# Optimization experiments

Hardware: AMD Instinct MI355X
Metric: run time of the kernel (lower is better)

The kernel has to match this reference:

```python
import jax, jax.numpy as jnp
import numpy as np

N_NODES = 50000
N_EDGES = 600000
N_COMM = 500
COMM_EDGES = 8000
NFEAT = 128
NHID = 128
NCLASS = 10
NLAYERS = 3
NHEADS = 8
EPS = 1e-5


def setup_inputs() -> dict:
    key = jax.random.key(0)
    ks = jax.random.split(key, 32)
    s = 0.05
    def rn(i, shape, scale=s):
        return (jax.random.normal(ks[i], shape, dtype=jnp.float32) * scale)
    return {
        "node_features": jax.random.normal(ks[0], (N_NODES, NFEAT), dtype=jnp.float32),
        "node_edge_index": jax.random.randint(ks[1], (2, N_EDGES), 0, N_NODES),
        "comm_features": jax.random.normal(ks[2], (N_COMM, NHID), dtype=jnp.float32),
        "comm_edge_index": jax.random.randint(ks[3], (2, COMM_EDGES), 0, N_COMM),
        "node_to_comm_map": jax.random.randint(ks[4], (N_NODES,), 0, N_COMM),
        # node-branch GCN params (nfeat == nhid so weights stack)
        "node_W": rn(5, (NLAYERS, NHID, NHID)),
        "node_b": rn(6, (NLAYERS, NHID)),
        "node_bn_g": 1.0 + rn(7, (NLAYERS, NHID)),
        "node_bn_b": rn(8, (NLAYERS, NHID)),
        # community-branch GCN params
        "comm_W": rn(9, (NLAYERS, NHID, NHID)),
        "comm_b": rn(10, (NLAYERS, NHID)),
        "comm_bn_g": 1.0 + rn(11, (NLAYERS, NHID)),
        "comm_bn_b": rn(12, (NLAYERS, NHID)),
        # MultiheadAttention params (torch layout: y = x @ W.T + b)
        "attn_in_w": rn(13, (3 * NHID, NHID)),
        "attn_in_b": rn(14, (3 * NHID,)),
        "attn_out_w": rn(15, (NHID, NHID)),
        "attn_out_b": rn(16, (NHID,)),
        # gate LayerNorm
        "ln_g": 1.0 + rn(17, (NHID,)),
        "ln_b": rn(18, (NHID,)),
        # classifier: Linear(128,64) -> BN -> ReLU -> Linear(64,10)
        "cls_W1": rn(19, (NHID, NHID // 2)),
        "cls_b1": rn(20, (NHID // 2,)),
        "cls_bn_g": 1.0 + rn(21, (NHID // 2,)),
        "cls_bn_b": rn(22, (NHID // 2,)),
        "cls_W2": rn(23, (NHID // 2, NCLASS)),
        "cls_b2": rn(24, (NCLASS,)),
    }


def _gcn_norm(edge_index, n):
    # PyG gcn_norm: add self-loops, symmetric D^-1/2 (A+I) D^-1/2
    loop = jnp.arange(n)
    src = jnp.concatenate([edge_index[0], loop])
    dst = jnp.concatenate([edge_index[1], loop])
    deg = jax.ops.segment_sum(jnp.ones(src.shape[0], jnp.float32), dst, num_segments=n)
    dinv = jnp.where(deg > 0, deg ** -0.5, 0.0)
    return src, dst, dinv[src] * dinv[dst]


def _gcn_stack(x, edge_index, Ws, bs, gs, betas):
    n = x.shape[0]
    src, dst, norm = _gcn_norm(edge_index, n)
    h = x
    for i in range(Ws.shape[0]):
        h_prev = h
        m = h @ Ws[i]  # linear commutes with normalized aggregation
        agg = jax.ops.segment_sum(m[src] * norm[:, None], dst, num_segments=n) + bs[i]
        mu = agg.mean(0)
        var = agg.var(0)  # biased, as torch BN training
        hb = (agg - mu) / jnp.sqrt(var + EPS) * gs[i] + betas[i]
        h = jax.nn.relu(hb)
        if i > 0:
            h = h + h_prev
    return h


def _mha(x, wi, bi, wo, bo):
    # x: [N, S=2, E]
    N, S, E = x.shape
    dh = E // NHEADS
    qkv = x @ wi.T + bi
    q, k, v = jnp.split(qkv, 3, axis=-1)
    q = q.reshape(N, S, NHEADS, dh)
    k = k.reshape(N, S, NHEADS, dh)
    v = v.reshape(N, S, NHEADS, dh)
    att = jnp.einsum('nqhd,nkhd->nhqk', q, k) / np.float32(np.sqrt(dh))
    att = jax.nn.softmax(att, axis=-1)
    o = jnp.einsum('nhqk,nkhd->nqhd', att, v).reshape(N, S, E)
    return o @ wo.T + bo


def reference(node_features, node_edge_index, comm_features, comm_edge_index,
              node_to_comm_map, node_W, node_b, node_bn_g, node_bn_b,
              comm_W, comm_b, comm_bn_g, comm_bn_b,
              attn_in_w, attn_in_b, attn_out_w, attn_out_b,
              ln_g, ln_b, cls_W1, cls_b1, cls_bn_g, cls_bn_b, cls_W2, cls_b2):
    h_node = _gcn_stack(node_features, node_edge_index, node_W, node_b, node_bn_g, node_bn_b)
    h_comm = _gcn_stack(comm_features, comm_edge_index, comm_W, comm_b, comm_bn_g, comm_bn_b)
    safe = jnp.clip(node_to_comm_map, 0, h_comm.shape[0] - 1)
    h_comm_exp = h_comm[safe]  # [N, nhid] cross-scale gather
    comb = jnp.stack([h_node, h_comm_exp], axis=1)  # [N, 2, nhid]
    attended = _mha(comb, attn_in_w, attn_in_b, attn_out_w, attn_out_b)
    x = attended.mean(axis=1) + h_node
    mu = x.mean(-1, keepdims=True)
    var = x.var(-1, keepdims=True)
    h_final = (x - mu) / jnp.sqrt(var + EPS) * ln_g + ln_b
    z = h_final @ cls_W1 + cls_b1
    zm = z.mean(0)
    zv = z.var(0)
    z = jax.nn.relu((z - zm) / jnp.sqrt(zv + EPS) * cls_bn_g + cls_bn_b)
    logits = z @ cls_W2 + cls_b2
    return jax.nn.log_softmax(logits, axis=-1)
```

## Files before the change

kernel.cpp:

```cpp
#include <hip/hip_runtime.h>
#include <hip/hip_bf16.h>
#include <cstdint>
#include <cstddef>


typedef __attribute__((ext_vector_type(8))) short bf16x8;
typedef __attribute__((ext_vector_type(4))) float f32x4;

#define EPSV 1e-5f

__device__ __forceinline__ float b2f(unsigned short u) {
    union { unsigned int i; float f; } x; x.i = ((unsigned int)u) << 16; return x.f;
}
__device__ __forceinline__ unsigned short f2b(float f) {
    union { float f; unsigned int i; } x; x.f = f;
    unsigned int i = x.i;
    return (unsigned short)((i + 0x7fffu + ((i >> 16) & 1u)) >> 16);
}

__global__ void prep_kernel(const float* __restrict__ node_W, const float* __restrict__ comm_W,
                            const float* __restrict__ cls_W1, const float* __restrict__ attn_in_w,
                            const float* __restrict__ attn_out_w, const float* __restrict__ comm_feat,
                            const float* __restrict__ node_feat,
                            unsigned short* __restrict__ WtN, unsigned short* __restrict__ WtC,
                            unsigned short* __restrict__ W1t, unsigned short* __restrict__ WinB,
                            unsigned short* __restrict__ WoutB, unsigned short* __restrict__ cfb,
                            unsigned short* __restrict__ nfb, int nC128, int nN128,
                            uint4* __restrict__ zreg, int zn4,
                            uint4* __restrict__ nreg, int nn4) {
    int idx = blockIdx.x * 256 + threadIdx.x;
    if (idx < 49152) {
        int l = idx >> 14, e = idx & 16383;
        int j = e & 7, lane = (e >> 3) & 63, kc = (e >> 9) & 3, t = e >> 11;
        int col = t * 16 + (lane & 15);
        int k = (lane >> 4) * 8 + kc * 32 + j;
        WtN[idx] = f2b(node_W[l * 16384 + k * 128 + col]); return;
    }
    idx -= 49152;
    if (idx < 49152) {
        int l = idx >> 14, e = idx & 16383;
        int j = e & 7, lane = (e >> 3) & 63, kc = (e >> 9) & 3, t = e >> 11;
        int col = t * 16 + (lane & 15);
        int k = (lane >> 4) * 8 + kc * 32 + j;
        WtC[idx] = f2b(comm_W[l * 16384 + k * 128 + col]); return;
    }
    idx -= 49152;
    if (idx < 8192) {
        int e = idx;
        int j = e & 7, lane = (e >> 3) & 63, kc = (e >> 9) & 3, t = e >> 11;
        int col = t * 16 + (lane & 15);
        int k = (lane >> 4) * 8 + kc * 32 + j;
        W1t[idx] = f2b(cls_W1[k * 64 + col]); return;
    }
    idx -= 8192;
    if (idx < 49152) {
        int e = idx;
        int j = e & 7, lane = (e >> 3) & 63, kc = (e >> 9) & 3, t = e >> 11;
        int col = t * 16 + (lane & 15);
        int k = (lane >> 4) * 8 + kc * 32 + j;
        WinB[idx] = f2b(attn_in_w[col * 128 + k]); return;
    }
    idx -= 49152;
    if (idx < 16384) {
        int e = idx;
        int j = e & 7, lane = (e >> 3) & 63, kc = (e >> 9) & 3, t = e >> 11;
        int col = t * 16 + (lane & 15);
        int k = (lane >> 4) * 8 + kc * 32 + j;
        WoutB[idx] = f2b(attn_out_w[col * 128 + k]); return;
    }
    idx -= 16384;
    if (idx < nC128) { cfb[idx] = f2b(comm_feat[idx]); return; }
    idx -= nC128;
    if (idx < nN128) { nfb[idx] = f2b(node_feat[idx]); return; }
    idx -= nN128;
    if (idx < zn4) { uint4 v; v.x = 0u; v.y = 0u; v.z = 0u; v.w = 0u; zreg[idx] = v; return; }
    idx -= zn4;
    if (idx < nn4) { uint4 v; v.x = 0xFFFFFFFFu; v.y = 0xFFFFFFFFu; v.z = 0xFFFFFFFFu; v.w = 0xFFFFFFFFu; nreg[idx] = v; }
}

__global__ void count_dual(const int* __restrict__ nd, int* __restrict__ cnt_n, int nE,
                           const int* __restrict__ cd, int* __restrict__ cnt_c, int cE) {
    int t = blockIdx.x * 256 + threadIdx.x;
    if (t < nE) atomicAdd(&cnt_n[nd[t]], 1);
    else if (t - nE < cE) atomicAdd(&cnt_c[cd[t - nE]], 1);
}

__global__ void scan_block_dual(const int* __restrict__ cnt_n, int* __restrict__ rs_n,
                                int* __restrict__ bsum_n, int nN, int nbN,
                                const int* __restrict__ cnt_c, int* __restrict__ rs_c,
                                int* __restrict__ bsum_c, int nC,
                                float* __restrict__ di_n, float* __restrict__ di_c) {
    __shared__ int tmp[2048];
    int nbC = (nC + 1023) >> 10;
    int extra = (int)blockIdx.x - (nbN + nbC);
    if (extra >= 0) {
        int g = extra * 1024 + (int)threadIdx.x;
        if (g < nN) di_n[g] = rsqrtf((float)cnt_n[g] + 1.0f);
        else { int gc = g - nN; if (gc < nC) di_c[gc] = rsqrtf((float)cnt_c[gc] + 1.0f); }
        return;
    }
    const int* cnt; int* excl; int* bsum; int n, lb;
    if ((int)blockIdx.x < nbN) { cnt = cnt_n; excl = rs_n; bsum = bsum_n; n = nN; lb = blockIdx.x; }
    else { cnt = cnt_c; excl = rs_c; bsum = bsum_c; n = nC; lb = blockIdx.x - nbN; }
    int tid = threadIdx.x;
    int gid = lb * 1024 + tid;
    int v = (gid < n) ? ((cnt[gid] + 7) & ~7) : 0;
    int buf = 0;
    tmp[tid] = v;
    __syncthreads();
    for (int d = 1; d < 1024; d <<= 1) {
        int t = tmp[buf * 1024 + tid];
        int add = (tid >= d) ? tmp[buf * 1024 + tid - d] : 0;
        tmp[(1 - buf) * 1024 + tid] = t + add;
        buf = 1 - buf;
        __syncthreads();
    }
    int inc = tmp[buf * 1024 + tid];
    if (gid < n) excl[gid] = inc - v;
    if (tid == 1023) bsum[lb] = inc;
}

__global__ void scan_add_dual(int* __restrict__ rs_n, const int* __restrict__ bsum_n,
                              int* __restrict__ cur_n, int nN,
                              int* __restrict__ rs_c, const int* __restrict__ bsum_c,
                              int* __restrict__ cur_c, int nC) {
    int gid = blockIdx.x * 256 + threadIdx.x;
    if (gid < nN) {
        int lb = gid >> 10;
        int p = 0;
        for (int i = 0; i < lb; ++i) p += bsum_n[i];
        int v = rs_n[gid] + p;
        rs_n[gid] = v; cur_n[gid] = v;
    } else {
        int g = gid - nN;
        if (g < nC) {
            int lb = g >> 10;
            int p = 0;
            for (int i = 0; i < lb; ++i) p += bsum_c[i];
            int v = rs_c[g] + p;
            rs_c[g] = v; cur_c[g] = v;
        }
    }
}

__device__ __forceinline__ void gemm_wave_128(const unsigned short* __restrict__ A,
                                              const unsigned short* __restrict__ Bt,
                                              const float* __restrict__ di,
                                              unsigned short* __restrict__ D,
                                              int M, int m0, int lane) {
    int r = lane & 15, q = lane >> 4;
    int arow = m0 + r; if (arow >= M) arow = M - 1;
    const unsigned short* ap = A + (size_t)arow * 128 + q * 8;
    bf16x8 afrag[4];
#pragma unroll
    for (int kc = 0; kc < 4; ++kc)
        afrag[kc] = *(const bf16x8*)(const void*)(ap + kc * 32);
    float dsc[4];
#pragma unroll
    for (int t = 0; t < 4; ++t) {
        int row = m0 + q * 4 + t; if (row >= M) row = M - 1;
        dsc[t] = di[row];
    }
#pragma unroll
    for (int tt = 0; tt < 8; ++tt) {
        f32x4 acc = {0.f, 0.f, 0.f, 0.f};
#pragma unroll
        for (int kc = 0; kc < 4; ++kc) {
            bf16x8 bfrag = *(const bf16x8*)(const void*)(Bt + (((size_t)tt * 4 + kc) << 9) + lane * 8);
            acc = __builtin_amdgcn_mfma_f32_16x16x32_bf16(afrag[kc], bfrag, acc, 0, 0, 0);
        }
        int n0 = tt * 16;
#pragma unroll
        for (int t = 0; t < 4; ++t) {
            int row = m0 + q * 4 + t;
            if (row < M) D[(size_t)row * 128 + n0 + r] = f2b(acc[t] * dsc[t]);
        }
    }
}

__global__ __launch_bounds__(256) void gemm_dual(
    const unsigned short* __restrict__ A0, const unsigned short* __restrict__ Bt0,
    const float* __restrict__ di0, unsigned short* __restrict__ D0, int M0, int blocksA,
    const unsigned short* __restrict__ A1, const unsigned short* __restrict__ Bt1,
    const float* __restrict__ di1, unsigned short* __restrict__ D1, int M1) {
    int blk = blockIdx.x;
    const unsigned short *A, *Bt; const float* di; unsigned short* D; int M, lb;
    if (blk < blocksA) { A = A0; Bt = Bt0; di = di0; D = D0; M = M0; lb = blk; }
    else { A = A1; Bt = Bt1; di = di1; D = D1; M = M1; lb = blk - blocksA; }
    int m0 = (lb * 4 + (int)(threadIdx.x >> 6)) * 16;
    if (m0 >= M) return;
    gemm_wave_128(A, Bt, di, D, M, m0, threadIdx.x & 63);
}

__global__ __launch_bounds__(256) void gemm_fill_kernel(
    const unsigned short* __restrict__ A0, const unsigned short* __restrict__ Bt0,
    const float* __restrict__ di0, unsigned short* __restrict__ D0, int M0, int blocksA,
    const unsigned short* __restrict__ A1, const unsigned short* __restrict__ Bt1,
    const float* __restrict__ di1, unsigned short* __restrict__ D1, int M1, int blocksB,
    const int* __restrict__ ns, const int* __restrict__ ndst,
    int* __restrict__ cur_n, int* __restrict__ csrc_n, int nE,
    const int* __restrict__ cs, const int* __restrict__ cdst,
    int* __restrict__ cur_c, int* __restrict__ csrc_c, int cE) {
    int blk = blockIdx.x;
    if (blk < blocksA + blocksB) {
        const unsigned short *A, *Bt; const float* di; unsigned short* D; int M, lb;
        if (blk < blocksA) { A = A0; Bt = Bt0; di = di0; D = D0; M = M0; lb = blk; }
        else { A = A1; Bt = Bt1; di = di1; D = D1; M = M1; lb = blk - blocksA; }
        int m0 = (lb * 4 + (int)(threadIdx.x >> 6)) * 16;
        if (m0 >= M) return;
        gemm_wave_128(A, Bt, di, D, M, m0, threadIdx.x & 63);
        return;
    }
    int e = (blk - blocksA - blocksB) * 256 + threadIdx.x;
    if (e < nE) {
        int s = ns[e], d = ndst[e];
        int pos = atomicAdd(&cur_n[d], 1);
        __builtin_nontemporal_store(s, csrc_n + pos);
    } else if (e - nE < cE) {
        int ee = e - nE;
        int s = cs[ee], d = cdst[ee];
        int pos = atomicAdd(&cur_c[d], 1);
        __builtin_nontemporal_store(s, csrc_c + pos);
    }
}

__global__ void gemm_kernel(const unsigned short* __restrict__ A,
                            const unsigned short* __restrict__ Bt,
                            const float* __restrict__ bias,
                            float* __restrict__ D, int M, int Ncol) {
    int wave = (blockIdx.x * blockDim.x + threadIdx.x) >> 6;
    int lane = threadIdx.x & 63;
    int m0 = wave * 16;
    if (m0 >= M) return;
    int r = lane & 15, q = lane >> 4;
    int arow = m0 + r; if (arow >= M) arow = M - 1;
    const unsigned short* ap = A + (size_t)arow * 128 + q * 8;
    bf16x8 afrag[4];
#pragma unroll
    for (int kc = 0; kc < 4; ++kc)
        afrag[kc] = *(const bf16x8*)(const void*)(ap + kc * 32);
    int ntiles = Ncol >> 4;
    for (int tt = 0; tt < ntiles; ++tt) {
        f32x4 acc = {0.f, 0.f, 0.f, 0.f};
#pragma unroll
        for (int kc = 0; kc < 4; ++kc) {
            bf16x8 bfrag = *(const bf16x8*)(const void*)(Bt + (((size_t)tt * 4 + kc) << 9) + lane * 8);
            acc = __builtin_amdgcn_mfma_f32_16x16x32_bf16(afrag[kc], bfrag, acc, 0, 0, 0);
        }
        int n0 = tt * 16;
        float bv = bias[n0 + r];
#pragma unroll
        for (int t = 0; t < 4; ++t) {
            int row = m0 + q * 4 + t;
            if (row < M) D[(size_t)row * Ncol + n0 + r] = acc[t] + bv;
        }
    }
}

__global__ __launch_bounds__(256) void gather_dual(
    const unsigned short* __restrict__ m0, const int* __restrict__ rs0,
    const int* __restrict__ cnt0, const int* __restrict__ cs0,
    const float* __restrict__ di0, const float* __restrict__ b0,
    float* __restrict__ agg0, float* __restrict__ bins0, int n0, int blocksA,
    const unsigned short* __restrict__ m1, const int* __restrict__ rs1,
    const int* __restrict__ cnt1, const int* __restrict__ cs1,
    const float* __restrict__ di1, const float* __restrict__ b1,
    float* __restrict__ agg1, float* __restrict__ bins1, int n1) {
    __shared__ float lsum[4][128], lsq[4][128];
    int blk = blockIdx.x;
    const unsigned short* m; const int *rs, *cnt, *cs; const float *di, *bias;
    float *agg, *bins; int n, lb;
    if (blk < blocksA) { m = m0; rs = rs0; cnt = cnt0; cs = cs0; di = di0; bias = b0; agg = agg0; bins = bins0; n = n0; lb = blk; }
    else { m = m1; rs = rs1; cnt = cnt1; cs = cs1; di = di1; bias = b1; agg = agg1; bins = bins1; n = n1; lb = blk - blocksA; }
    int wib = threadIdx.x >> 6, lane = threadIdx.x & 63;
    int node = lb * 4 + wib;
    bool act = node < n;
    float a0 = 0.f, a1 = 0.f;
    if (act) {
        int start = rs[node];
        int end = start + ((cnt[node] + 7) & ~7);
        for (int i = start; i < end; i += 8) {
            int s[8]; unsigned int v[8];
#pragma unroll
            for (int j = 0; j < 8; ++j) s[j] = cs[i + j];
#pragma unroll
            for (int j = 0; j < 8; ++j) {
                int si = s[j] < 0 ? node : s[j];
                v[j] = *(const unsigned int*)(m + (size_t)si * 128 + 2 * lane);
            }
#pragma unroll
            for (int j = 0; j < 8; ++j) {
                float wj = s[j] >= 0 ? 1.f : 0.f;
                a0 += b2f((unsigned short)(v[j] & 0xffff)) * wj;
                a1 += b2f((unsigned short)(v[j] >> 16)) * wj;
            }
        }
        unsigned int v = *(const unsigned int*)(m + (size_t)node * 128 + 2 * lane);
        a0 += b2f((unsigned short)(v & 0xffff));
        a1 += b2f((unsigned short)(v >> 16));
        float d = di[node];
        a0 = a0 * d + bias[2 * lane];
        a1 = a1 * d + bias[2 * lane + 1];
        float2 o; o.x = a0; o.y = a1;
        ((float2*)(agg + (size_t)node * 128))[lane] = o;
    }
    lsum[wib][2 * lane] = a0;       lsum[wib][2 * lane + 1] = a1;
    lsq[wib][2 * lane] = a0 * a0;   lsq[wib][2 * lane + 1] = a1 * a1;
    __syncthreads();
    int t = threadIdx.x;
    int bb = (lb & 31) * 256;
    if (t < 128) {
        float v = lsum[0][t] + lsum[1][t] + lsum[2][t] + lsum[3][t];
        atomicAdd(&bins[bb + t], v);
    } else {
        int c = t - 128;
        float v = lsq[0][c] + lsq[1][c] + lsq[2][c] + lsq[3][c];
        atomicAdd(&bins[bb + 128 + c], v);
    }
}

__global__ void stats_fin_dual(float* __restrict__ bins0, float* __restrict__ s0,
                               float* __restrict__ bins1, float* __restrict__ s1) {
    int t = threadIdx.x;
    float a = 0.f;
#pragma unroll
    for (int b = 0; b < 32; ++b) { a += bins0[b * 256 + t]; bins0[b * 256 + t] = 0.f; }
    s0[t] = a;
    float c = 0.f;
#pragma unroll
    for (int b = 0; b < 32; ++b) { c += bins1[b * 256 + t]; bins1[b * 256 + t] = 0.f; }
    s1[t] = c;
}

__global__ __launch_bounds__(256) void apply_dual(
    const float* __restrict__ agg0, const float* __restrict__ sums0,
    const float* __restrict__ g0, const float* __restrict__ be0,
    unsigned short* __restrict__ hb0, int n0, int blocksA, int useRes,
    const float* __restrict__ agg1, const float* __restrict__ sums1,
    const float* __restrict__ g1, const float* __restrict__ be1,
    unsigned short* __restrict__ hb1, int n1) {
    __shared__ float sc[128], sh[128];
    int blk = blockIdx.x;
    const float *agg, *sums, *g, *be; unsigned short* hb; int n, lb;
    if (blk < blocksA) { agg = agg0; sums = sums0; g = g0; be = be0; hb = hb0; n = n0; lb = blk; }
    else { agg = agg1; sums = sums1; g = g1; be = be1; hb = hb1; n = n1; lb = blk - blocksA; }
    int t = threadIdx.x;
    if (t < 128) {
        float inv = 1.f / (float)n;
        float mean = sums[t] * inv;
        float var = sums[128 + t] * inv - mean * mean;
        float rstd = rsqrtf(var + EPSV);
        float s = g[t] * rstd;
        sc[t] = s;
        sh[t] = be[t] - mean * s;
    }
    __syncthreads();
    int base = lb * 1024 + t * 4;
    if (base < n * 128) {
        float4 a = *(const float4*)(agg + base);
        ushort4 h = *(const ushort4*)(hb + base);
        int f = base & 127;
        float v0 = fmaxf(a.x * sc[f] + sh[f], 0.f);
        float v1 = fmaxf(a.y * sc[f + 1] + sh[f + 1], 0.f);
        float v2 = fmaxf(a.z * sc[f + 2] + sh[f + 2], 0.f);
        float v3 = fmaxf(a.w * sc[f + 3] + sh[f + 3], 0.f);
        if (useRes) { v0 += b2f(h.x); v1 += b2f(h.y); v2 += b2f(h.z); v3 += b2f(h.w); }
        ushort4 o; o.x = f2b(v0); o.y = f2b(v1); o.z = f2b(v2); o.w = f2b(v3);
        *(ushort4*)(hb + base) = o;
    }
}

__global__ __launch_bounds__(256) void mha_fused_kernel(
    const unsigned short* __restrict__ hbn, const int* __restrict__ map,
    const float* __restrict__ cqkv,
    const unsigned short* __restrict__ WinB, const float* __restrict__ bin,
    const unsigned short* __restrict__ WoutB, const float* __restrict__ bout,
    const float* __restrict__ lng, const float* __restrict__ lnb,
    const unsigned short* __restrict__ W1t, const float* __restrict__ b1v,
    float* __restrict__ z, float* __restrict__ zbins, int nN, int nC) {
    __shared__ unsigned short obf_s[16 * 144];
    __shared__ float att_s[16 * 132];

    int b = blockIdx.x;
    int hg = threadIdx.x >> 6;
    int lane = threadIdx.x & 63;
    int r = lane & 15, q = lane >> 4;

    int arow = b * 16 + r; if (arow >= nN) arow = nN - 1;
    const unsigned short* ap = hbn + (size_t)arow * 128 + q * 8;
    bf16x8 afrag[4];
#pragma unroll
    for (int kc = 0; kc < 4; ++kc)
        afrag[kc] = *(const bf16x8*)(const void*)(ap + kc * 32);

    const float* cp[4];
#pragma unroll
    for (int t = 0; t < 4; ++t) {
        int nt = b * 16 + q * 4 + t; if (nt >= nN) nt = nN - 1;
        int c = map[nt]; c = c < 0 ? 0 : (c >= nC ? nC - 1 : c);
        cp[t] = cqkv + (size_t)c * 384;
    }

#pragma unroll
    for (int c = 0; c < 2; ++c) {
        int h = hg * 2 + c;
        f32x4 qa, ka, va;
#pragma unroll
        for (int p = 0; p < 3; ++p) {
            int tt = p * 8 + h;
            f32x4 acc = {0.f, 0.f, 0.f, 0.f};
#pragma unroll
            for (int kc = 0; kc < 4; ++kc) {
                bf16x8 bfrag = *(const bf16x8*)(const void*)(WinB + (((size_t)tt * 4 + kc) << 9) + lane * 8);
                acc = __builtin_amdgcn_mfma_f32_16x16x32_bf16(afrag[kc], bfrag, acc, 0, 0, 0);
            }
            float bv = bin[tt * 16 + r];
#pragma unroll
            for (int t = 0; t < 4; ++t) acc[t] += bv;
            if (p == 0) qa = acc; else if (p == 1) ka = acc; else va = acc;
        }
        float qc[4], kc_[4], vc[4];
#pragma unroll
        for (int t = 0; t < 4; ++t) {
            const float* cpt = cp[t] + h * 16 + r;
            qc[t] = cpt[0]; kc_[t] = cpt[128]; vc[t] = cpt[256];
        }
#pragma unroll
        for (int t = 0; t < 4; ++t) {
            float s00 = qa[t] * ka[t];
            float s01 = qa[t] * kc_[t];
            float s10 = qc[t] * ka[t];
            float s11 = qc[t] * kc_[t];
#pragma unroll
            for (int mku = 1; mku <= 8; mku <<= 1) {
                s00 += __shfl_xor(s00, mku); s01 += __shfl_xor(s01, mku);
                s10 += __shfl_xor(s10, mku); s11 += __shfl_xor(s11, mku);
            }
            s00 *= 0.25f; s01 *= 0.25f; s10 *= 0.25f; s11 *= 0.25f;
            float m0 = fmaxf(s00, s01), m1 = fmaxf(s10, s11);
            float e00 = __expf(s00 - m0), e01 = __expf(s01 - m0);
            float e10 = __expf(s10 - m1), e11 = __expf(s11 - m1);
            float i0 = 1.f / (e00 + e01), i1 = 1.f / (e10 + e11);
            float o0 = (e00 * va[t] + e01 * vc[t]) * i0;
            float o1 = (e10 * va[t] + e11 * vc[t]) * i1;
            obf_s[(q * 4 + t) * 144 + h * 16 + r] = f2b(0.5f * (o0 + o1));
        }
    }
    __syncthreads();

    bf16x8 ofrag[4];
#pragma unroll
    for (int kc = 0; kc < 4; ++kc)
        ofrag[kc] = *(const bf16x8*)(const void*)(obf_s + r * 144 + q * 8 + kc * 32);
#pragma unroll
    for (int c = 0; c < 2; ++c) {
        int tt = hg * 2 + c;
        f32x4 acc = {0.f, 0.f, 0.f, 0.f};
#pragma unroll
        for (int kc = 0; kc < 4; ++kc) {
            bf16x8 bfrag = *(const bf16x8*)(const void*)(WoutB + (((size_t)tt * 4 + kc) << 9) + lane * 8);
            acc = __builtin_amdgcn_mfma_f32_16x16x32_bf16(ofrag[kc], bfrag, acc, 0, 0, 0);
        }
        int n0 = tt * 16;
        float bv = bout[n0 + r];
#pragma unroll
        for (int t = 0; t < 4; ++t)
            att_s[(q * 4 + t) * 132 + n0 + r] = acc[t] + bv;
    }
    __syncthreads();
    unsigned short* hf_s = obf_s;

    {
        int nl = threadIdx.x >> 4;
        int j = threadIdx.x & 15;
        int gnode = b * 16 + nl;
        if (gnode >= nN) gnode = nN - 1;
        const unsigned short* hrow = hbn + (size_t)gnode * 128 + j * 8;
        ushort4 ha = *(const ushort4*)(hrow);
        ushort4 hbv = *(const ushort4*)(hrow + 4);
        float x[8]; float s = 0.f, s2 = 0.f;
        x[0] = att_s[nl * 132 + j * 8 + 0] + b2f(ha.x);
        x[1] = att_s[nl * 132 + j * 8 + 1] + b2f(ha.y);
        x[2] = att_s[nl * 132 + j * 8 + 2] + b2f(ha.z);
        x[3] = att_s[nl * 132 + j * 8 + 3] + b2f(ha.w);
        x[4] = att_s[nl * 132 + j * 8 + 4] + b2f(hbv.x);
        x[5] = att_s[nl * 132 + j * 8 + 5] + b2f(hbv.y);
        x[6] = att_s[nl * 132 + j * 8 + 6] + b2f(hbv.z);
        x[7] = att_s[nl * 132 + j * 8 + 7] + b2f(hbv.w);
#pragma unroll
        for (int i = 0; i < 8; ++i) { s += x[i]; s2 += x[i] * x[i]; }
        s += __shfl_xor(s, 1);  s2 += __shfl_xor(s2, 1);
        s += __shfl_xor(s, 2);  s2 += __shfl_xor(s2, 2);
        s += __shfl_xor(s, 4);  s2 += __shfl_xor(s2, 4);
        s += __shfl_xor(s, 8);  s2 += __shfl_xor(s2, 8);
        float mu = s * (1.f / 128.f);
        float var = s2 * (1.f / 128.f) - mu * mu;
        float rstd = rsqrtf(var + EPSV);
        ushort4 o1, o2;
        o1.x = f2b((x[0] - mu) * rstd * lng[j * 8 + 0] + lnb[j * 8 + 0]);
        o1.y = f2b((x[1] - mu) * rstd * lng[j * 8 + 1] + lnb[j * 8 + 1]);
        o1.z = f2b((x[2] - mu) * rstd * lng[j * 8 + 2] + lnb[j * 8 + 2]);
        o1.w = f2b((x[3] - mu) * rstd * lng[j * 8 + 3] + lnb[j * 8 + 3]);
        o2.x = f2b((x[4] - mu) * rstd * lng[j * 8 + 4] + lnb[j * 8 + 4]);
        o2.y = f2b((x[5] - mu) * rstd * lng[j * 8 + 5] + lnb[j * 8 + 5]);
        o2.z = f2b((x[6] - mu) * rstd * lng[j * 8 + 6] + lnb[j * 8 + 6]);
        o2.w = f2b((x[7] - mu) * rstd * lng[j * 8 + 7] + lnb[j * 8 + 7]);
        *(ushort4*)(hf_s + nl * 136 + j * 8) = o1;
        *(ushort4*)(hf_s + nl * 136 + j * 8 + 4) = o2;
    }
    __syncthreads();

    {
        bf16x8 hfrag[4];
#pragma unroll
        for (int kc = 0; kc < 4; ++kc)
            hfrag[kc] = *(const bf16x8*)(const void*)(hf_s + r * 136 + q * 8 + kc * 32);
        f32x4 acc = {0.f, 0.f, 0.f, 0.f};
#pragma unroll
        for (int kc = 0; kc < 4; ++kc) {
            bf16x8 bfrag = *(const bf16x8*)(const void*)(W1t + (((size_t)hg * 4 + kc) << 9) + lane * 8);
            acc = __builtin_amdgcn_mfma_f32_16x16x32_bf16(hfrag[kc], bfrag, acc, 0, 0, 0);
        }
        float bv = b1v[hg * 16 + r];
        float s = 0.f, s2 = 0.f;
#pragma unroll
        for (int t = 0; t < 4; ++t) {
            int row = b * 16 + q * 4 + t;
            if (row < nN) {
                float v = acc[t] + bv;
                z[(size_t)row * 64 + hg * 16 + r] = v;
                s += v; s2 += v * v;
            }
        }
        s += __shfl_xor(s, 16);  s2 += __shfl_xor(s2, 16);
        s += __shfl_xor(s, 32);  s2 += __shfl_xor(s2, 32);
        if (lane < 16) {
            int bb = (b & 31) * 128;
            atomicAdd(&zbins[bb + hg * 16 + r], s);
            atomicAdd(&zbins[bb + 64 + hg * 16 + r], s2);
        }
    }
}

__global__ void stats_fin_z(const float* __restrict__ bins, float* __restrict__ s) {
    int t = threadIdx.x;
    float a = 0.f;
#pragma unroll
    for (int b = 0; b < 32; ++b) a += bins[b * 128 + t];
    s[t] = a;
}

__global__ __launch_bounds__(256) void final_kernel(const float* __restrict__ z,
                                                    const float* __restrict__ sums,
                                                    const float* __restrict__ g,
                                                    const float* __restrict__ be,
                                                    const float* __restrict__ W2,
                                                    const float* __restrict__ b2v,
                                                    float* __restrict__ out, int nN) {
    int node = blockIdx.x * 4 + (threadIdx.x >> 6);
    int lane = threadIdx.x & 63;
    float inv = 1.f / (float)nN;
    float mean = sums[lane] * inv;
    float var = sums[64 + lane] * inv - mean * mean;
    float sc = g[lane] * rsqrtf(var + EPSV);
    float sh = be[lane] - mean * sc;
    float v = 0.f;
    if (node < nN) v = fmaxf(z[(size_t)node * 64 + lane] * sc + sh, 0.f);
    float p[10];
    const float* wrow = W2 + lane * 10;
#pragma unroll
    for (int c = 0; c < 10; ++c) p[c] = v * wrow[c];
#pragma unroll
    for (int off = 32; off >= 1; off >>= 1) {
#pragma unroll
        for (int c = 0; c < 10; ++c) p[c] += __shfl_xor(p[c], off);
    }
    if (node >= nN) return;
    float l[10], mx = -1e30f;
#pragma unroll
    for (int c = 0; c < 10; ++c) { l[c] = p[c] + b2v[c]; mx = fmaxf(mx, l[c]); }
    float se = 0.f;
#pragma unroll
    for (int c = 0; c < 10; ++c) se += expf(l[c] - mx);
    float lse = mx + logf(se);
    if (lane < 10) out[(size_t)node * 10 + lane] = l[lane] - lse;
}

static inline int cdiv(long a, long b) { return (int)((a + b - 1) / b); }

extern "C" void kernel_launch(void* const* d_in, const int* in_sizes, int n_in,
                              void* d_out, int out_size, void* d_ws, size_t ws_size,
                              hipStream_t stream) {
    const float* node_feat = (const float*)d_in[0];
    const int*   nedge     = (const int*)d_in[1];
    const float* comm_feat = (const float*)d_in[2];
    const int*   cedge     = (const int*)d_in[3];
    const int*   n2c       = (const int*)d_in[4];
    const float* node_W    = (const float*)d_in[5];
    const float* node_b    = (const float*)d_in[6];
    const float* node_g    = (const float*)d_in[7];
    const float* node_beta = (const float*)d_in[8];
    const float* comm_W    = (const float*)d_in[9];
    const float* comm_b    = (const float*)d_in[10];
    const float* comm_g    = (const float*)d_in[11];
    const float* comm_beta = (const float*)d_in[12];
    const float* attn_in_w = (const float*)d_in[13];
    const float* attn_in_b = (const float*)d_in[14];
    const float* attn_out_w= (const float*)d_in[15];
    const float* attn_out_b= (const float*)d_in[16];
    const float* ln_g      = (const float*)d_in[17];
    const float* ln_b      = (const float*)d_in[18];
    const float* cls_W1    = (const float*)d_in[19];
    const float* cls_b1    = (const float*)d_in[20];
    const float* cls_bn_g  = (const float*)d_in[21];
    const float* cls_bn_b  = (const float*)d_in[22];
    const float* cls_W2    = (const float*)d_in[23];
    const float* cls_b2    = (const float*)d_in[24];

    const int nN = in_sizes[0] / 128;
    const int nE = in_sizes[1] / 2;
    const int nC = in_sizes[2] / 128;
    const int cE = in_sizes[3] / 2;
    const int padE_n = nE + 8 * nN;
    const int padE_c = cE + 8 * nC;

    char* ws = (char*)d_ws;
    size_t off = 0;
    auto alloc = [&](size_t bytes) -> char* {
        char* p = ws + off;
        off = (off + bytes + 255) & ~(size_t)255;
        return p;
    };
    size_t zero_begin = off;
    int*   cnt_n  = (int*)alloc((size_t)nN * 4);
    int*   cur_n  = (int*)alloc((size_t)nN * 4);
    int*   cnt_c  = (int*)alloc((size_t)nC * 4);
    int*   cur_c  = (int*)alloc((size_t)nC * 4);
    float* gsums  = (float*)alloc((size_t)6 * 256 * 4);
    float* csums  = (float*)alloc(128 * 4);
    float* bins_n = (float*)alloc((size_t)32 * 256 * 4);
    float* bins_c = (float*)alloc((size_t)32 * 256 * 4);
    float* zbins  = (float*)alloc((size_t)32 * 128 * 4);
    size_t zero_bytes = off - zero_begin;
    size_t neg_begin = off;
    int*   csrc_n = (int*)alloc((size_t)padE_n * 4);
    int*   csrc_c = (int*)alloc((size_t)padE_c * 4);
    size_t neg_bytes = off - neg_begin;
    int*   rs_n   = (int*)alloc((size_t)(nN + 1) * 4);
    int*   bsum_n = (int*)alloc(256 * 4);
    float* dinv_n = (float*)alloc((size_t)nN * 4);
    int*   rs_c   = (int*)alloc((size_t)(nC + 1) * 4);
    int*   bsum_c = (int*)alloc(256 * 4);
    float* dinv_c = (float*)alloc((size_t)nC * 4);
    unsigned short* hb_n  = (unsigned short*)alloc((size_t)nN * 256);
    unsigned short* hb_c  = (unsigned short*)alloc((size_t)nC * 256);
    unsigned short* cfb   = (unsigned short*)alloc((size_t)nC * 256);
    unsigned short* m_cb  = (unsigned short*)alloc((size_t)nC * 256);
    float*          agg_c = (float*)alloc((size_t)nC * 512);
    float*          cqkv  = (float*)alloc((size_t)nC * 384 * 4);
    unsigned short* WtN  = (unsigned short*)alloc((size_t)3 * 16384 * 2);
    unsigned short* WtC  = (unsigned short*)alloc((size_t)3 * 16384 * 2);
    unsigned short* W1t  = (unsigned short*)alloc((size_t)64 * 128 * 2);
    unsigned short* WinB = (unsigned short*)alloc((size_t)384 * 128 * 2);
    unsigned short* WoutB= (unsigned short*)alloc((size_t)128 * 128 * 2);
    unsigned short* m_nb = (unsigned short*)alloc((size_t)nN * 256);
    float*          agg_n= (float*)alloc((size_t)nN * 512);
    unsigned short* nfb  = (unsigned short*)agg_n;
    float*          z    = agg_n;

    int zn4 = (int)(zero_bytes / 16);
    int nn4 = (int)(neg_bytes / 16);
    long prepN = 49152L * 3 + 8192 + 16384 + (long)nC * 128 + (long)nN * 128;
    long prepTotal = prepN + zn4 + nn4;
    prep_kernel<<<cdiv(prepTotal, 256), 256, 0, stream>>>(
        node_W, comm_W, cls_W1, attn_in_w, attn_out_w, comm_feat, node_feat,
        WtN, WtC, W1t, WinB, WoutB, cfb, nfb, nC * 128, nN * 128,
        (uint4*)(ws + zero_begin), zn4, (uint4*)(ws + neg_begin), nn4);

    count_dual<<<cdiv((long)nE + cE, 256), 256, 0, stream>>>(nedge + nE, cnt_n, nE, cedge + cE, cnt_c, cE);
    int nbN = cdiv(nN, 1024), nbC = cdiv(nC, 1024);
    int dinvB = cdiv((long)nN + nC, 1024);
    scan_block_dual<<<nbN + nbC + dinvB, 1024, 0, stream>>>(
        cnt_n, rs_n, bsum_n, nN, nbN, cnt_c, rs_c, bsum_c, nC, dinv_n, dinv_c);
    scan_add_dual<<<cdiv((long)nN + nC, 256), 256, 0, stream>>>(
        rs_n, bsum_n, cur_n, nN, rs_c, bsum_c, cur_c, nC);

    int gemmA = cdiv(nN, 64), gemmB = cdiv(nC, 64);
    int fillB = cdiv((long)nE + cE, 256);
    int gatA = cdiv(nN, 4), gatB = cdiv(nC, 4);
    int appA = cdiv((long)nN * 128, 1024), appB = cdiv((long)nC * 128, 1024);
    for (int i = 0; i < 3; ++i) {
        float* s0 = gsums + (size_t)(i * 2 + 0) * 256;
        float* s1 = gsums + (size_t)(i * 2 + 1) * 256;
        if (i == 0) {
            gemm_fill_kernel<<<gemmA + gemmB + fillB, 256, 0, stream>>>(
                nfb, WtN, dinv_n, m_nb, nN, gemmA,
                cfb, WtC, dinv_c, m_cb, nC, gemmB,
                nedge, nedge + nE, cur_n, csrc_n, nE,
                cedge, cedge + cE, cur_c, csrc_c, cE);
        } else {
            gemm_dual<<<gemmA + gemmB, 256, 0, stream>>>(
                hb_n, WtN + i * 16384, dinv_n, m_nb, nN, gemmA,
                hb_c, WtC + i * 16384, dinv_c, m_cb, nC);
        }
        gather_dual<<<gatA + gatB, 256, 0, stream>>>(
            m_nb, rs_n, cnt_n, csrc_n, dinv_n, node_b + i * 128, agg_n, bins_n, nN, gatA,
            m_cb, rs_c, cnt_c, csrc_c, dinv_c, comm_b + i * 128, agg_c, bins_c, nC);
        stats_fin_dual<<<1, 256, 0, stream>>>(bins_n, s0, bins_c, s1);
        apply_dual<<<appA + appB, 256, 0, stream>>>(
            agg_n, s0, node_g + i * 128, node_beta + i * 128, hb_n, nN, appA, i > 0 ? 1 : 0,
            agg_c, s1, comm_g + i * 128, comm_beta + i * 128, hb_c, nC);
    }

    int cwaves = cdiv(nC, 16);
    gemm_kernel<<<cdiv((long)cwaves * 64, 256), 256, 0, stream>>>(
        hb_c, WinB, attn_in_b, cqkv, nC, 384);

    mha_fused_kernel<<<cdiv(nN, 16), 256, 0, stream>>>(
        hb_n, n2c, cqkv, WinB, attn_in_b, WoutB, attn_out_b, ln_g, ln_b,
        W1t, cls_b1, z, zbins, nN, nC);

    stats_fin_z<<<1, 128, 0, stream>>>(zbins, csums);
    final_kernel<<<cdiv(nN, 4), 256, 0, stream>>>(z, csums, cls_bn_g, cls_bn_b,
                                                  cls_W2, cls_b2, (float*)d_out, nN);
}
```

Baseline: 477.0 us.

## Fold stats-finalize and count kernels into neighbors to cut launches

Removes the separate single-block stats_fin_dual, stats_fin_z and count_dual launches. Each apply/final block now reduces the 32 partial bins itself, with per-layer bin buffers so no re-zeroing is needed. Edge-degree counting is merged into prep_kernel, and zeroing moves to hipMemsetAsync. apply and final blocks also handle four times more work each, which cuts block count but makes every block redundantly re-read the bins.

```diff
diff --git a/kernel.cpp b/kernel.cpp
--- a/kernel.cpp
+++ b/kernel.cpp
@@ -26,8 +26,9 @@
                             unsigned short* __restrict__ W1t, unsigned short* __restrict__ WinB,
                             unsigned short* __restrict__ WoutB, unsigned short* __restrict__ cfb,
                             unsigned short* __restrict__ nfb, int nC128, int nN128,
-                            uint4* __restrict__ zreg, int zn4,
-                            uint4* __restrict__ nreg, int nn4) {
+                            uint4* __restrict__ nreg, int nn4,
+                            const int* __restrict__ ndst, int* __restrict__ cnt_n, int nE,
+                            const int* __restrict__ cdst, int* __restrict__ cnt_c, int cE) {
     int idx = blockIdx.x * 256 + threadIdx.x;
     if (idx < 49152) {
         int l = idx >> 14, e = idx & 16383;
@@ -73,16 +74,14 @@
     idx -= nC128;
     if (idx < nN128) { nfb[idx] = f2b(node_feat[idx]); return; }
     idx -= nN128;
-    if (idx < zn4) { uint4 v; v.x = 0u; v.y = 0u; v.z = 0u; v.w = 0u; zreg[idx] = v; return; }
-    idx -= zn4;
-    if (idx < nn4) { uint4 v; v.x = 0xFFFFFFFFu; v.y = 0xFFFFFFFFu; v.z = 0xFFFFFFFFu; v.w = 0xFFFFFFFFu; nreg[idx] = v; }
-}
-
-__global__ void count_dual(const int* __restrict__ nd, int* __restrict__ cnt_n, int nE,
-                           const int* __restrict__ cd, int* __restrict__ cnt_c, int cE) {
-    int t = blockIdx.x * 256 + threadIdx.x;
-    if (t < nE) atomicAdd(&cnt_n[nd[t]], 1);
-    else if (t - nE < cE) atomicAdd(&cnt_c[cd[t - nE]], 1);
+    if (idx < nn4) {
+        uint4 v; v.x = 0xFFFFFFFFu; v.y = 0xFFFFFFFFu; v.z = 0xFFFFFFFFu; v.w = 0xFFFFFFFFu;
+        nreg[idx] = v; return;
+    }
+    idx -= nn4;
+    if (idx < nE) { atomicAdd(&cnt_n[ndst[idx]], 1); return; }
+    idx -= nE;
+    if (idx < cE) atomicAdd(&cnt_c[cdst[idx]], 1);
 }
 
 __global__ void scan_block_dual(const int* __restrict__ cnt_n, int* __restrict__ rs_n,
@@ -319,54 +318,51 @@
     }
 }
 
-__global__ void stats_fin_dual(float* __restrict__ bins0, float* __restrict__ s0,
-                               float* __restrict__ bins1, float* __restrict__ s1) {
-    int t = threadIdx.x;
-    float a = 0.f;
-#pragma unroll
-    for (int b = 0; b < 32; ++b) { a += bins0[b * 256 + t]; bins0[b * 256 + t] = 0.f; }
-    s0[t] = a;
-    float c = 0.f;
-#pragma unroll
-    for (int b = 0; b < 32; ++b) { c += bins1[b * 256 + t]; bins1[b * 256 + t] = 0.f; }
-    s1[t] = c;
-}
-
 __global__ __launch_bounds__(256) void apply_dual(
-    const float* __restrict__ agg0, const float* __restrict__ sums0,
+    const float* __restrict__ agg0, const float* __restrict__ bins0,
     const float* __restrict__ g0, const float* __restrict__ be0,
     unsigned short* __restrict__ hb0, int n0, int blocksA, int useRes,
-    const float* __restrict__ agg1, const float* __restrict__ sums1,
+    const float* __restrict__ agg1, const float* __restrict__ bins1,
     const float* __restrict__ g1, const float* __restrict__ be1,
     unsigned short* __restrict__ hb1, int n1) {
-    __shared__ float sc[128], sh[128];
+    __shared__ float sc[128], sh[128], bs[256];
     int blk = blockIdx.x;
-    const float *agg, *sums, *g, *be; unsigned short* hb; int n, lb;
-    if (blk < blocksA) { agg = agg0; sums = sums0; g = g0; be = be0; hb = hb0; n = n0; lb = blk; }
-    else { agg = agg1; sums = sums1; g = g1; be = be1; hb = hb1; n = n1; lb = blk - blocksA; }
+    const float *agg, *bins, *g, *be; unsigned short* hb; int n, lb;
+    if (blk < blocksA) { agg = agg0; bins = bins0; g = g0; be = be0; hb = hb0; n = n0; lb = blk; }
+    else { agg = agg1; bins = bins1; g = g1; be = be1; hb = hb1; n = n1; lb = blk - blocksA; }
     int t = threadIdx.x;
+    {
+        float a = 0.f;
+#pragma unroll
+        for (int b = 0; b < 32; ++b) a += bins[b * 256 + t];
+        bs[t] = a;
+    }
+    __syncthreads();
     if (t < 128) {
         float inv = 1.f / (float)n;
-        float mean = sums[t] * inv;
-        float var = sums[128 + t] * inv - mean * mean;
+        float mean = bs[t] * inv;
+        float var = bs[128 + t] * inv - mean * mean;
         float rstd = rsqrtf(var + EPSV);
         float s = g[t] * rstd;
         sc[t] = s;
         sh[t] = be[t] - mean * s;
     }
     __syncthreads();
-    int base = lb * 1024 + t * 4;
-    if (base < n * 128) {
-        float4 a = *(const float4*)(agg + base);
-        ushort4 h = *(const ushort4*)(hb + base);
-        int f = base & 127;
-        float v0 = fmaxf(a.x * sc[f] + sh[f], 0.f);
-        float v1 = fmaxf(a.y * sc[f + 1] + sh[f + 1], 0.f);
-        float v2 = fmaxf(a.z * sc[f + 2] + sh[f + 2], 0.f);
-        float v3 = fmaxf(a.w * sc[f + 3] + sh[f + 3], 0.f);
-        if (useRes) { v0 += b2f(h.x); v1 += b2f(h.y); v2 += b2f(h.z); v3 += b2f(h.w); }
-        ushort4 o; o.x = f2b(v0); o.y = f2b(v1); o.z = f2b(v2); o.w = f2b(v3);
-        *(ushort4*)(hb + base) = o;
+#pragma unroll
+    for (int it = 0; it < 4; ++it) {
+        int base = (lb * 4 + it) * 1024 + t * 4;
+        if (base < n * 128) {
+            float4 a = *(const float4*)(agg + base);
+            ushort4 h = *(const ushort4*)(hb + base);
+            int f = base & 127;
+            float v0 = fmaxf(a.x * sc[f] + sh[f], 0.f);
+            float v1 = fmaxf(a.y * sc[f + 1] + sh[f + 1], 0.f);
+            float v2 = fmaxf(a.z * sc[f + 2] + sh[f + 2], 0.f);
+            float v3 = fmaxf(a.w * sc[f + 3] + sh[f + 3], 0.f);
+            if (useRes) { v0 += b2f(h.x); v1 += b2f(h.y); v2 += b2f(h.z); v3 += b2f(h.w); }
+            ushort4 o; o.x = f2b(v0); o.y = f2b(v1); o.z = f2b(v2); o.w = f2b(v3);
+            *(ushort4*)(hb + base) = o;
+        }
     }
 }
 
@@ -542,48 +538,53 @@
     }
 }
 
-__global__ void stats_fin_z(const float* __restrict__ bins, float* __restrict__ s) {
-    int t = threadIdx.x;
-    float a = 0.f;
-#pragma unroll
-    for (int b = 0; b < 32; ++b) a += bins[b * 128 + t];
-    s[t] = a;
-}
-
 __global__ __launch_bounds__(256) void final_kernel(const float* __restrict__ z,
-                                                    const float* __restrict__ sums,
+                                                    const float* __restrict__ zbins,
                                                     const float* __restrict__ g,
                                                     const float* __restrict__ be,
                                                     const float* __restrict__ W2,
                                                     const float* __restrict__ b2v,
                                                     float* __restrict__ out, int nN) {
-    int node = blockIdx.x * 4 + (threadIdx.x >> 6);
-    int lane = threadIdx.x & 63;
+    __shared__ float zs[128];
+    int t = threadIdx.x;
+    if (t < 128) {
+        float a = 0.f;
+#pragma unroll
+        for (int b = 0; b < 32; ++b) a += zbins[b * 128 + t];
+        zs[t] = a;
+    }
+    __syncthreads();
+    int lane = t & 63;
     float inv = 1.f / (float)nN;
-    float mean = sums[lane] * inv;
-    float var = sums[64 + lane] * inv - mean * mean;
+    float mean = zs[lane] * inv;
+    float var = zs[64 + lane] * inv - mean * mean;
     float sc = g[lane] * rsqrtf(var + EPSV);
     float sh = be[lane] - mean * sc;
-    float v = 0.f;
-    if (node < nN) v = fmaxf(z[(size_t)node * 64 + lane] * sc + sh, 0.f);
-    float p[10];
     const float* wrow = W2 + lane * 10;
 #pragma unroll
-    for (int c = 0; c < 10; ++c) p[c] = v * wrow[c];
-#pragma unroll
-    for (int off = 32; off >= 1; off >>= 1) {
-#pragma unroll
-        for (int c = 0; c < 10; ++c) p[c] += __shfl_xor(p[c], off);
-    }
-    if (node >= nN) return;
-    float l[10], mx = -1e30f;
-#pragma unroll
-    for (int c = 0; c < 10; ++c) { l[c] = p[c] + b2v[c]; mx = fmaxf(mx, l[c]); }
-    float se = 0.f;
-#pragma unroll
-    for (int c = 0; c < 10; ++c) se += expf(l[c] - mx);
-    float lse = mx + logf(se);
-    if (lane < 10) out[(size_t)node * 10 + lane] = l[lane] - lse;
+    for (int it = 0; it < 4; ++it) {
+        int node = blockIdx.x * 16 + (t >> 6) * 4 + it;
+        float v = 0.f;
+        if (node < nN) v = fmaxf(z[(size_t)node * 64 + lane] * sc + sh, 0.f);
+        float p[10];
+#pragma unroll
+        for (int c = 0; c < 10; ++c) p[c] = v * wrow[c];
+#pragma unroll
+        for (int off = 32; off >= 1; off >>= 1) {
+#pragma unroll
+            for (int c = 0; c < 10; ++c) p[c] += __shfl_xor(p[c], off);
+        }
+        if (node < nN) {
+            float l[10], mx = -1e30f;
+#pragma unroll
+            for (int c = 0; c < 10; ++c) { l[c] = p[c] + b2v[c]; mx = fmaxf(mx, l[c]); }
+            float se = 0.f;
+#pragma unroll
+            for (int c = 0; c < 10; ++c) se += expf(l[c] - mx);
+            float lse = mx + logf(se);
+            if (lane < 10) out[(size_t)node * 10 + lane] = l[lane] - lse;
+        }
+    }
 }
 
 static inline int cdiv(long a, long b) { return (int)((a + b - 1) / b); }
@@ -636,10 +637,8 @@
     int*   cur_n  = (int*)alloc((size_t)nN * 4);
     int*   cnt_c  = (int*)alloc((size_t)nC * 4);
     int*   cur_c  = (int*)alloc((size_t)nC * 4);
-    float* gsums  = (float*)alloc((size_t)6 * 256 * 4);
-    float* csums  = (float*)alloc(128 * 4);
-    float* bins_n = (float*)alloc((size_t)32 * 256 * 4);
-    float* bins_c = (float*)alloc((size_t)32 * 256 * 4);
+    float* bins_n = (float*)alloc((size_t)3 * 32 * 256 * 4);
+    float* bins_c = (float*)alloc((size_t)3 * 32 * 256 * 4);
     float* zbins  = (float*)alloc((size_t)32 * 128 * 4);
     size_t zero_bytes = off - zero_begin;
     size_t neg_begin = off;
@@ -668,16 +667,17 @@
     unsigned short* nfb  = (unsigned short*)agg_n;
     float*          z    = agg_n;
 
-    int zn4 = (int)(zero_bytes / 16);
+    hipMemsetAsync(ws + zero_begin, 0, zero_bytes, stream);
+
     int nn4 = (int)(neg_bytes / 16);
     long prepN = 49152L * 3 + 8192 + 16384 + (long)nC * 128 + (long)nN * 128;
-    long prepTotal = prepN + zn4 + nn4;
+    long prepTotal = prepN + nn4 + nE + cE;
     prep_kernel<<<cdiv(prepTotal, 256), 256, 0, stream>>>(
         node_W, comm_W, cls_W1, attn_in_w, attn_out_w, comm_feat, node_feat,
         WtN, WtC, W1t, WinB, WoutB, cfb, nfb, nC * 128, nN * 128,
-        (uint4*)(ws + zero_begin), zn4, (uint4*)(ws + neg_begin), nn4);
-
-    count_dual<<<cdiv((long)nE + cE, 256), 256, 0, stream>>>(nedge + nE, cnt_n, nE, cedge + cE, cnt_c, cE);
+        (uint4*)(ws + neg_begin), nn4,
+        nedge + nE, cnt_n, nE, cedge + cE, cnt_c, cE);
+
     int nbN = cdiv(nN, 1024), nbC = cdiv(nC, 1024);
     int dinvB = cdiv((long)nN + nC, 1024);
     scan_block_dual<<<nbN + nbC + dinvB, 1024, 0, stream>>>(
@@ -688,10 +688,10 @@
     int gemmA = cdiv(nN, 64), gemmB = cdiv(nC, 64);
     int fillB = cdiv((long)nE + cE, 256);
     int gatA = cdiv(nN, 4), gatB = cdiv(nC, 4);
-    int appA = cdiv((long)nN * 128, 1024), appB = cdiv((long)nC * 128, 1024);
+    int appA = cdiv((long)nN * 128, 4096), appB = cdiv((long)nC * 128, 4096);
     for (int i = 0; i < 3; ++i) {
-        float* s0 = gsums + (size_t)(i * 2 + 0) * 256;
-        float* s1 = gsums + (size_t)(i * 2 + 1) * 256;
+        float* bn_i = bins_n + (size_t)i * 32 * 256;
+        float* bc_i = bins_c + (size_t)i * 32 * 256;
         if (i == 0) {
             gemm_fill_kernel<<<gemmA + gemmB + fillB, 256, 0, stream>>>(
                 nfb, WtN, dinv_n, m_nb, nN, gemmA,
@@ -704,12 +704,11 @@
                 hb_c, WtC + i * 16384, dinv_c, m_cb, nC);
         }
         gather_dual<<<gatA + gatB, 256, 0, stream>>>(
-            m_nb, rs_n, cnt_n, csrc_n, dinv_n, node_b + i * 128, agg_n, bins_n, nN, gatA,
-            m_cb, rs_c, cnt_c, csrc_c, dinv_c, comm_b + i * 128, agg_c, bins_c, nC);
-        stats_fin_dual<<<1, 256, 0, stream>>>(bins_n, s0, bins_c, s1);
+            m_nb, rs_n, cnt_n, csrc_n, dinv_n, node_b + i * 128, agg_n, bn_i, nN, gatA,
+            m_cb, rs_c, cnt_c, csrc_c, dinv_c, comm_b + i * 128, agg_c, bc_i, nC);
         apply_dual<<<appA + appB, 256, 0, stream>>>(
-            agg_n, s0, node_g + i * 128, node_beta + i * 128, hb_n, nN, appA, i > 0 ? 1 : 0,
-            agg_c, s1, comm_g + i * 128, comm_beta + i * 128, hb_c, nC);
+            agg_n, bn_i, node_g + i * 128, node_beta + i * 128, hb_n, nN, appA, i > 0 ? 1 : 0,
+            agg_c, bc_i, comm_g + i * 128, comm_beta + i * 128, hb_c, nC);
     }
 
     int cwaves = cdiv(nC, 16);
@@ -720,7 +719,6 @@
         hb_n, n2c, cqkv, WinB, attn_in_b, WoutB, attn_out_b, ln_g, ln_b,
         W1t, cls_b1, z, zbins, nN, nC);
 
-    stats_fin_z<<<1, 128, 0, stream>>>(zbins, csums);
-    final_kernel<<<cdiv(nN, 4), 256, 0, stream>>>(z, csums, cls_bn_g, cls_bn_b,
-                                                  cls_W2, cls_b2, (float*)d_out, nN);
-}
+    final_kernel<<<cdiv(nN, 16), 256, 0, stream>>>(
+        z, zbins, cls_bn_g, cls_bn_b, cls_W2, cls_b2, (float*)d_out, nN);
+}
```

Result: no change. 468.7 us (-1.7%).
